# Optimization experiments

Measured on AMD Instinct MI355X. Metric: run time of the kernel, lower is better.

Reference implementation:

```python
import jax, jax.numpy as jnp
import numpy as np

N_VERTICES = 1_000_000
N_EDGES = 16_000_000


def setup_inputs() -> dict:
    key = jax.random.key(0)
    k1, k2, k3, k4 = jax.random.split(key, 4)
    # vertex_attr columns: [A_ii, b_i, x_i]; A_ii kept positive & away from 0
    A_ii = jax.random.uniform(k1, (N_VERTICES, 1), dtype=jnp.float32) + 0.5
    b_i = jax.random.normal(k2, (N_VERTICES, 1), dtype=jnp.float32)
    x_i = jax.random.normal(k3, (N_VERTICES, 1), dtype=jnp.float32)
    vertex_attr = jnp.concatenate([A_ii, b_i, x_i], axis=1)
    edgeij_pair = jax.random.randint(k4, (2, N_EDGES), 0, N_VERTICES, dtype=jnp.int64 if jax.config.read('jax_enable_x64') else jnp.int32)
    edge_attr = jax.random.normal(jax.random.fold_in(key, 5), (N_EDGES, 1), dtype=jnp.float32) * 0.05
    g = jnp.array([0.6667], dtype=jnp.float32)  # Jacobi damping weight w = g[0]
    batch = jnp.zeros((N_VERTICES,), dtype=edgeij_pair.dtype)  # single graph
    return {"vertex_attr": vertex_attr, "edgeij_pair": edgeij_pair,
            "edge_attr": edge_attr, "g": g, "batch": batch}


def reference(vertex_attr, edgeij_pair, edge_attr, g, batch):
    n = vertex_attr.shape[0]
    A_ii = vertex_attr[:, 0:1]  # [N,1]
    b_i = vertex_attr[:, 1:2]
    x_i = vertex_attr[:, 2:3]
    w = g[0]
    # edge-to-vertex scatter-sum aggregation: cbar_i = sum_{j in N(i)} c_ij
    dst = edgeij_pair[0]
    cbar_i = jax.ops.segment_sum(edge_attr[:, 0], dst, num_segments=n)[:, None]  # [N,1]
    # damped Jacobi update
    x_new = x_i + w * (b_i - cbar_i) / A_ii
    return jnp.concatenate([A_ii, b_i, x_new], axis=1)
```

## Files before the change

### kernel.cpp

```cpp
#include <hip/hip_runtime.h>

#define TPB    256
#define VSHIFT 12
#define VBUCK  (1 << VSHIFT)
#define NBMAX  256
#define EPT    16
#define ROUND  (TPB * EPT)
#define RPB    4
#define PBLK   (ROUND * RPB)
#define SPLITMAX 4
#define ATPB   1024
#define KDEP   8

#define FPSCALE20  1048576.0f
#define FPINV20    9.5367431640625e-7f

typedef unsigned uint32x4 __attribute__((ext_vector_type(4)));

__device__ __forceinline__ unsigned pack_edge(int d, float v) {
    int fix = __float2int_rn(v * FPSCALE20);
    return ((unsigned)(d & (VBUCK - 1)) << 20) | ((unsigned)fix & 0xFFFFFu);
}

__device__ __forceinline__ uint32x4 gload16_async(const void* p) {
    uint32x4 r;
    asm volatile("global_load_dwordx4 %0, %1, off"
                 : "=&v"(r) : "v"(p));
    return r;
}

__device__ __forceinline__ int block_excl_scan(int v, int t, int* wsum, int* total) {
    int s = v;
    #pragma unroll
    for (int d = 1; d < 64; d <<= 1) {
        int u = __shfl_up(s, d);
        if ((t & 63) >= d) s += u;
    }
    if ((t & 63) == 63) wsum[t >> 6] = s;
    __syncthreads();
    int add = 0;
    #pragma unroll
    for (int w = 0; w < TPB / 64; ++w)
        if (w < (t >> 6)) add += wsum[w];
    int tot = wsum[0] + wsum[1] + wsum[2] + wsum[3];
    __syncthreads();
    *total = tot;
    return s + add - v;
}

__global__ void hist_rounds_kernel(const int* __restrict__ dst, long long n_edge,
                                   int nblk, int* __restrict__ histp_t,
                                   int* __restrict__ histp_b) {
    __shared__ int h[NBMAX];
    const int t = threadIdx.x;
    const long long bbase = (long long)blockIdx.x * PBLK;
    int total = 0;
    for (int r = 0; r < RPB; ++r) {
        h[t] = 0;
        __syncthreads();
        const long long rbase = bbase + (long long)r * ROUND;
        #pragma unroll
        for (int j = 0; j < EPT / 4; ++j) {
            long long e = rbase + ((long long)j * TPB + t) * 4;
            if (e + 4 <= n_edge) {
                int4 d = *reinterpret_cast<const int4*>(dst + e);
                atomicAdd(&h[d.x >> VSHIFT], 1);
                atomicAdd(&h[d.y >> VSHIFT], 1);
                atomicAdd(&h[d.z >> VSHIFT], 1);
                atomicAdd(&h[d.w >> VSHIFT], 1);
            } else {
                for (int q = 0; q < 4; ++q) {
                    long long ee = e + q;
                    if (ee < n_edge) atomicAdd(&h[dst[ee] >> VSHIFT], 1);
                }
            }
        }
        __syncthreads();
        int hv = h[t];
        histp_t[((size_t)blockIdx.x * RPB + r) * NBMAX + t] = hv;
        total += hv;
    }
    histp_b[(size_t)t * nblk + blockIdx.x] = total;
}

__global__ void row_scan_kernel(int* __restrict__ histp, int nblk,
                                int* __restrict__ totals) {
    __shared__ int wsum[TPB / 64];
    const int t = threadIdx.x;
    int* row = histp + (size_t)blockIdx.x * nblk;
    int carry = 0;
    for (int base = 0; base < nblk; base += TPB) {
        int v = (base + t < nblk) ? row[base + t] : 0;
        int tot;
        int excl = block_excl_scan(v, t, wsum, &tot);
        if (base + t < nblk) row[base + t] = carry + excl;
        carry += tot;
        __syncthreads();
    }
    if (t == 0) totals[blockIdx.x] = carry;
}

__global__ void base_scan_kernel(const int* __restrict__ totals, int nb,
                                 int* __restrict__ base) {
    __shared__ int wsum[TPB / 64];
    const int t = threadIdx.x;
    int v = (t < nb) ? totals[t] : 0;
    int tot;
    int excl = block_excl_scan(v, t, wsum, &tot);
    base[t] = excl;
    if (t == TPB - 1) base[TPB] = excl + v;
}

__global__ __launch_bounds__(TPB, 7)
void partition_kernel(const int* __restrict__ dst,
                      const float* __restrict__ ea,
                      long long n_edge, int nblk,
                      const int* __restrict__ histp_t,
                      const int* __restrict__ histp_b,
                      const int* __restrict__ base,
                      unsigned* __restrict__ pairs) {
    __shared__ unsigned      stage[ROUND];
    __shared__ unsigned char stage_b[ROUND];
    __shared__ int pos[NBMAX];
    __shared__ int adj[NBMAX];
    __shared__ int wsum[TPB / 64];

    const int t = threadIdx.x;
    const long long bbase = (long long)blockIdx.x * PBLK;
    int my_gbase = base[t] + histp_b[(size_t)t * nblk + blockIdx.x];

    int hv[RPB];
    #pragma unroll
    for (int r = 0; r < RPB; ++r)
        hv[r] = histp_t[((size_t)blockIdx.x * RPB + r) * NBMAX + t];

    if (bbase + PBLK <= n_edge) {
        int4   dr[2][EPT / 4];
        float4 vr[2][EPT / 4];
        #pragma unroll
        for (int j = 0; j < EPT / 4; ++j) {
            long long e = bbase + ((long long)j * TPB + t) * 4;
            dr[0][j] = *reinterpret_cast<const int4*>(dst + e);
            vr[0][j] = *reinterpret_cast<const float4*>(ea + e);
        }
        #pragma unroll
        for (int r = 0; r < RPB; ++r) {
            const int cur = r & 1, nxt = cur ^ 1;
            if (r + 1 < RPB) {
                const long long pb = bbase + (long long)(r + 1) * ROUND;
                #pragma unroll
                for (int j = 0; j < EPT / 4; ++j) {
                    long long e = pb + ((long long)j * TPB + t) * 4;
                    dr[nxt][j] = *reinterpret_cast<const int4*>(dst + e);
                    vr[nxt][j] = *reinterpret_cast<const float4*>(ea + e);
                }
            }
            int rt;
            int excl = block_excl_scan(hv[r], t, wsum, &rt);
            pos[t] = excl;
            adj[t] = my_gbase - excl;
            __syncthreads();
            #pragma unroll
            for (int j = 0; j < EPT / 4; ++j) {
                int   dd[4] = {dr[cur][j].x, dr[cur][j].y, dr[cur][j].z, dr[cur][j].w};
                float vv[4] = {vr[cur][j].x, vr[cur][j].y, vr[cur][j].z, vr[cur][j].w};
                #pragma unroll
                for (int q = 0; q < 4; ++q) {
                    int b = dd[q] >> VSHIFT;
                    int slot = atomicAdd(&pos[b], 1);
                    stage[slot]   = pack_edge(dd[q], vv[q]);
                    stage_b[slot] = (unsigned char)b;
                }
            }
            __syncthreads();
            #pragma unroll
            for (int i0 = 0; i0 < ROUND; i0 += TPB) {
                int i = i0 + t;
                unsigned p = stage[i];
                int b = stage_b[i];
                pairs[(size_t)(adj[b] + i)] = p;
            }
            my_gbase += hv[r];
        }
    } else {
        const long long bend = n_edge;
        for (int r = 0; r < RPB; ++r) {
            const long long rbase = bbase + (long long)r * ROUND;
            if (rbase >= bend) break;

            int4   dreg[EPT / 4];
            float4 vreg[EPT / 4];
            int    nval[EPT / 4];
            #pragma unroll
            for (int j = 0; j < EPT / 4; ++j) {
                long long e = rbase + ((long long)j * TPB + t) * 4;
                if (e + 4 <= bend) {
                    dreg[j] = *reinterpret_cast<const int4*>(dst + e);
                    vreg[j] = *reinterpret_cast<const float4*>(ea + e);
                    nval[j] = 4;
                } else {
                    int dd[4] = {0, 0, 0, 0};
                    float vv[4] = {0.f, 0.f, 0.f, 0.f};
                    int nv = 0;
                    for (int q = 0; q < 4; ++q) {
                        long long ee = e + q;
                        if (ee < bend) { dd[q] = dst[ee]; vv[q] = ea[ee]; nv = q + 1; }
                    }
                    dreg[j] = make_int4(dd[0], dd[1], dd[2], dd[3]);
                    vreg[j] = make_float4(vv[0], vv[1], vv[2], vv[3]);
                    nval[j] = nv;
                }
            }

            int rt;
            int excl = block_excl_scan(hv[r], t, wsum, &rt);
            pos[t] = excl;
            adj[t] = my_gbase - excl;
            __syncthreads();

            #pragma unroll
            for (int j = 0; j < EPT / 4; ++j) {
                int   dd[4] = {dreg[j].x, dreg[j].y, dreg[j].z, dreg[j].w};
                float vv[4] = {vreg[j].x, vreg[j].y, vreg[j].z, vreg[j].w};
                #pragma unroll
                for (int q = 0; q < 4; ++q) {
                    if (q < nval[j]) {
                        int b = dd[q] >> VSHIFT;
                        int slot = atomicAdd(&pos[b], 1);
                        stage[slot]   = pack_edge(dd[q], vv[q]);
                        stage_b[slot] = (unsigned char)b;
                    }
                }
            }
            __syncthreads();

            for (int i = t; i < rt; i += TPB) {
                unsigned p = stage[i];
                int b = stage_b[i];
                pairs[(size_t)(adj[b] + i)] = p;
            }
            __syncthreads();
            my_gbase += hv[r];
        }
    }
}

__global__ __launch_bounds__(ATPB)
void accum_partial_kernel(const unsigned* pairs,
                          const int* __restrict__ base,
                          float* __restrict__ partials, int n_vert, int nb,
                          int split) {
    __shared__ __align__(16) int acc[VBUCK];
    const int b  = blockIdx.x % nb;
    const int sp = blockIdx.x / nb;
    const int t  = threadIdx.x;
    #pragma unroll
    for (int i = t; i < VBUCK; i += ATPB) acc[i] = 0;
    __syncthreads();

    const int s = base[b];
    const int e = base[b + 1];
    const long long len = e - s;
    const int i0 = s + (int)((len * sp) / split);
    const int i1 = s + (int)((len * (sp + 1)) / split);
    int a0 = (i0 + 3) & ~3;
    if (a0 > i1) a0 = i1;
    const int a1 = a0 + (((i1 - a0) >> 2) << 2);

    if (t == 0) {
        for (int i = i0; i < a0; ++i) {
            unsigned p = pairs[i];
            atomicAdd(&acc[(int)(p >> 20)], ((int)(p << 12)) >> 12);
        }
    }
    if (t == 1) {
        for (int i = a1; i < i1; ++i) {
            unsigned p = pairs[i];
            atomicAdd(&acc[(int)(p >> 20)], ((int)(p << 12)) >> 12);
        }
    }

    const int n4 = (a1 - a0) >> 2;
    if (n4 > 0) {
        const char* pv = reinterpret_cast<const char*>(pairs + a0);
        const int nm1 = n4 - 1;
        for (int bb = 0; bb < n4; bb += KDEP * ATPB) {
            uint32x4 q[KDEP];
            int idx[KDEP];
            #pragma unroll
            for (int k = 0; k < KDEP; ++k) {
                idx[k] = bb + t + k * ATPB;
                int ci = idx[k] < nm1 ? idx[k] : nm1;
                q[k] = gload16_async(pv + (size_t)ci * 16);
            }
            asm volatile("s_waitcnt vmcnt(0)" ::: "memory");
            __builtin_amdgcn_sched_barrier(0);
            #pragma unroll
            for (int k = 0; k < KDEP; ++k) {
                if (idx[k] < n4) {
                    #pragma unroll
                    for (int u = 0; u < 4; ++u) {
                        unsigned p = q[k][u];
                        atomicAdd(&acc[(int)(p >> 20)], ((int)(p << 12)) >> 12);
                    }
                }
            }
        }
    }
    __syncthreads();

    float* pp = partials + (size_t)sp * n_vert;
    const int vbase = b << VSHIFT;
    if (vbase + VBUCK <= n_vert) {
        int4 a = reinterpret_cast<const int4*>(acc)[t];
        float4 f;
        f.x = (float)a.x * FPINV20; f.y = (float)a.y * FPINV20;
        f.z = (float)a.z * FPINV20; f.w = (float)a.w * FPINV20;
        reinterpret_cast<float4*>(pp + vbase)[t] = f;
    } else {
        for (int v = t; vbase + v < n_vert; v += ATPB)
            pp[vbase + v] = (float)acc[v] * FPINV20;
    }
}

__global__ void final_update_kernel(const float* __restrict__ partials,
                                    const float* __restrict__ va,
                                    const float* __restrict__ g,
                                    float* __restrict__ out, int n_vert,
                                    int split) {
    const int gt = blockIdx.x * blockDim.x + threadIdx.x;
    const float w = g[0];
    const int v0 = gt * 4;
    if (v0 + 4 <= n_vert) {
        float4 c = reinterpret_cast<const float4*>(partials)[gt];
        for (int sp = 1; sp < split; ++sp) {
            float4 c2 = reinterpret_cast<const float4*>(
                            partials + (size_t)sp * n_vert)[gt];
            c.x += c2.x; c.y += c2.y; c.z += c2.z; c.w += c2.w;
        }
        float4 f0 = reinterpret_cast<const float4*>(va)[gt * 3 + 0];
        float4 f1 = reinterpret_cast<const float4*>(va)[gt * 3 + 1];
        float4 f2 = reinterpret_cast<const float4*>(va)[gt * 3 + 2];
        float4 o0, o1, o2;
        o0.x = f0.x; o0.y = f0.y; o0.z = f0.z + w * (f0.y - c.x) / f0.x;
        o0.w = f0.w; o1.x = f1.x; o1.y = f1.y + w * (f1.x - c.y) / f0.w;
        o1.z = f1.z; o1.w = f1.w; o2.x = f2.x + w * (f1.w - c.z) / f1.z;
        o2.y = f2.y; o2.z = f2.z; o2.w = f2.w + w * (f2.z - c.w) / f2.y;
        reinterpret_cast<float4*>(out)[gt * 3 + 0] = o0;
        reinterpret_cast<float4*>(out)[gt * 3 + 1] = o1;
        reinterpret_cast<float4*>(out)[gt * 3 + 2] = o2;
    } else {
        for (int i = v0; i < n_vert; ++i) {
            float c = 0.f;
            for (int sp = 0; sp < split; ++sp)
                c += partials[(size_t)sp * n_vert + i];
            float A = va[3 * i], bb = va[3 * i + 1], x = va[3 * i + 2];
            out[3 * i]     = A;
            out[3 * i + 1] = bb;
            out[3 * i + 2] = x + w * (bb - c) / A;
        }
    }
}

__global__ void accum_update_kernel(const unsigned* __restrict__ pairs,
                                    const int* __restrict__ base,
                                    const float* __restrict__ va,
                                    const float* __restrict__ g,
                                    float* __restrict__ out, int n_vert) {
    __shared__ __align__(16) int acc[VBUCK];
    const int b = blockIdx.x;
    const int T = blockDim.x;
    for (int t = threadIdx.x; t < VBUCK; t += T) acc[t] = 0;
    __syncthreads();
    const int s = base[b];
    const int e = base[b + 1];
    for (int i = s + threadIdx.x; i < e; i += T) {
        unsigned p = pairs[i];
        atomicAdd(&acc[(int)(p >> 20)], ((int)(p << 12)) >> 12);
    }
    __syncthreads();

    const float w = g[0];
    const int vbase = b << VSHIFT;
    const int t = threadIdx.x;
    const int v0 = vbase + t * 4;
    if (v0 + 4 <= n_vert) {
        const int gt = v0 >> 2;
        float4 f0 = reinterpret_cast<const float4*>(va)[gt * 3 + 0];
        float4 f1 = reinterpret_cast<const float4*>(va)[gt * 3 + 1];
        float4 f2 = reinterpret_cast<const float4*>(va)[gt * 3 + 2];
        int4   a  = reinterpret_cast<const int4*>(acc)[t];
        float4 c;
        c.x = (float)a.x * FPINV20; c.y = (float)a.y * FPINV20;
        c.z = (float)a.z * FPINV20; c.w = (float)a.w * FPINV20;
        float4 o0, o1, o2;
        o0.x = f0.x; o0.y = f0.y; o0.z = f0.z + w * (f0.y - c.x) / f0.x;
        o0.w = f0.w; o1.x = f1.x; o1.y = f1.y + w * (f1.x - c.y) / f0.w;
        o1.z = f1.z; o1.w = f1.w; o2.x = f2.x + w * (f1.w - c.z) / f1.z;
        o2.y = f2.y; o2.z = f2.z; o2.w = f2.w + w * (f2.z - c.w) / f2.y;
        reinterpret_cast<float4*>(out)[gt * 3 + 0] = o0;
        reinterpret_cast<float4*>(out)[gt * 3 + 1] = o1;
        reinterpret_cast<float4*>(out)[gt * 3 + 2] = o2;
    } else {
        for (int i = v0; i < n_vert && i < v0 + 4; ++i) {
            float A = va[3 * i], bb = va[3 * i + 1], x = va[3 * i + 2];
            out[3 * i]     = A;
            out[3 * i + 1] = bb;
            out[3 * i + 2] = x + w * (bb - (float)acc[i - vbase] * FPINV20) / A;
        }
    }
}

__global__ void scatter_add_dev_kernel(const int* __restrict__ dst,
                                       const float* __restrict__ ea,
                                       float* __restrict__ acc, int n_edges4) {
    int i = blockIdx.x * blockDim.x + threadIdx.x;
    const int stride = gridDim.x * blockDim.x;
    for (; i < n_edges4; i += stride) {
        int4   d = reinterpret_cast<const int4*>(dst)[i];
        float4 v = reinterpret_cast<const float4*>(ea)[i];
        atomicAdd(&acc[d.x], v.x);
        atomicAdd(&acc[d.y], v.y);
        atomicAdd(&acc[d.z], v.z);
        atomicAdd(&acc[d.w], v.w);
    }
}

__global__ void update_kernel(const float* __restrict__ va,
                              const float* __restrict__ cbar,
                              const float* __restrict__ g,
                              float* __restrict__ out, int n) {
    int i = blockIdx.x * blockDim.x + threadIdx.x;
    if (i >= n) return;
    float A = va[3 * i], b = va[3 * i + 1], x = va[3 * i + 2];
    out[3 * i]     = A;
    out[3 * i + 1] = b;
    out[3 * i + 2] = x + g[0] * (b - cbar[i]) / A;
}

extern "C" void kernel_launch(void* const* d_in, const int* in_sizes, int n_in,
                              void* d_out, int out_size, void* d_ws, size_t ws_size,
                              hipStream_t stream) {
    const float* vertex_attr = (const float*)d_in[0];
    const int*   edgeij      = (const int*)d_in[1];
    const float* edge_attr   = (const float*)d_in[2];
    const float* g           = (const float*)d_in[3];

    const int       n_vert = in_sizes[0] / 3;
    const long long n_edge = in_sizes[2];
    const int       nb     = (n_vert + VBUCK - 1) >> VSHIFT;
    const int       nblk   = (int)((n_edge + PBLK - 1) / PBLK);

    size_t histt_sz   = (size_t)nblk * RPB * NBMAX * sizeof(int);
    size_t histb_off  = (histt_sz + 255) & ~(size_t)255;
    size_t histb_sz   = (size_t)NBMAX * nblk * sizeof(int);
    size_t totals_off = (histb_off + histb_sz + 255) & ~(size_t)255;
    size_t base_off   = totals_off + NBMAX * sizeof(int);
    size_t pairs_off  = (base_off + (TPB + 1) * sizeof(int) + 255) & ~(size_t)255;
    size_t need1      = pairs_off + (size_t)n_edge * sizeof(unsigned);
    size_t part_off   = (need1 + 255) & ~(size_t)255;

    if (ws_size >= need1 && nb <= NBMAX) {
        int* histp_t = (int*)d_ws;
        int* histp_b = (int*)((char*)d_ws + histb_off);
        int* totals  = (int*)((char*)d_ws + totals_off);
        int* basep   = (int*)((char*)d_ws + base_off);
        unsigned* pairs = (unsigned*)((char*)d_ws + pairs_off);

        hist_rounds_kernel<<<nblk, TPB, 0, stream>>>(edgeij, n_edge, nblk,
                                                     histp_t, histp_b);
        row_scan_kernel<<<nb, TPB, 0, stream>>>(histp_b, nblk, totals);
        base_scan_kernel<<<1, TPB, 0, stream>>>(totals, nb, basep);
        partition_kernel<<<nblk, TPB, 0, stream>>>(edgeij, edge_attr, n_edge,
                                                   nblk, histp_t, histp_b,
                                                   basep, pairs);

        int split = 0;
        for (int sp = SPLITMAX; sp >= 2; sp >>= 1) {
            if (ws_size >= part_off + (size_t)sp * n_vert * sizeof(float)) {
                split = sp; break;
            }
        }
        if (split) {
            float* partials = (float*)((char*)d_ws + part_off);
            accum_partial_kernel<<<nb * split, ATPB, 0, stream>>>(
                pairs, basep, partials, n_vert, nb, split);
            const int uthreads = (n_vert + 3) / 4;
            final_update_kernel<<<(uthreads + TPB - 1) / TPB, TPB, 0, stream>>>(
                partials, vertex_attr, g, (float*)d_out, n_vert, split);
        } else {
            accum_update_kernel<<<nb, 1024, 0, stream>>>(pairs, basep, vertex_attr,
                                                         g, (float*)d_out, n_vert);
        }
    } else {
        float* cbar = (float*)d_ws;
        hipMemsetAsync(cbar, 0, (size_t)n_vert * sizeof(float), stream);
        scatter_add_dev_kernel<<<4096, TPB, 0, stream>>>(edgeij, edge_attr, cbar,
                                                         (int)(n_edge / 4));
        update_kernel<<<(n_vert + TPB - 1) / TPB, TPB, 0, stream>>>(
            vertex_attr, cbar, g, (float*)d_out, n_vert);
    }
}
```

Measured before the change: 127.0 us.

## Pad each bucket run in partitioned edge pairs to 8-element alignment

Each per-round, per-bucket segment of the partitioned pair array is rounded up to a multiple of 8 entries, and the gaps are filled with zero-valued dummy entries (packed 0 adds nothing to the accumulation). The aim is aligned 32-byte runs so that the scattered global writes and later reads of pairs are better coalesced or vector-aligned. In exchange the stage buffer grows (STG), occupancy hint drops from 7 to 5 blocks, the pairs array is larger, and the extra padding entries add memory traffic.

```diff
diff --git a/kernel.cpp b/kernel.cpp
--- a/kernel.cpp
+++ b/kernel.cpp
@@ -11,11 +11,17 @@
 #define SPLITMAX 4
 #define ATPB   1024
 #define KDEP   8
+#define PADE   8
+#define STG    5824
 
 #define FPSCALE20  1048576.0f
 #define FPINV20    9.5367431640625e-7f
 
 typedef unsigned uint32x4 __attribute__((ext_vector_type(4)));
+
+__device__ __host__ __forceinline__ int padup(int h) {
+    return h ? ((h + PADE - 1) & ~(PADE - 1)) : 0;
+}
 
 __device__ __forceinline__ unsigned pack_edge(int d, float v) {
     int fix = __float2int_rn(v * FPSCALE20);
@@ -78,7 +84,7 @@
         __syncthreads();
         int hv = h[t];
         histp_t[((size_t)blockIdx.x * RPB + r) * NBMAX + t] = hv;
-        total += hv;
+        total += padup(hv);
     }
     histp_b[(size_t)t * nblk + blockIdx.x] = total;
 }
@@ -111,7 +117,7 @@
     if (t == TPB - 1) base[TPB] = excl + v;
 }
 
-__global__ __launch_bounds__(TPB, 7)
+__global__ __launch_bounds__(TPB, 5)
 void partition_kernel(const int* __restrict__ dst,
                       const float* __restrict__ ea,
                       long long n_edge, int nblk,
@@ -119,8 +125,8 @@
                       const int* __restrict__ histp_b,
                       const int* __restrict__ base,
                       unsigned* __restrict__ pairs) {
-    __shared__ unsigned      stage[ROUND];
-    __shared__ unsigned char stage_b[ROUND];
+    __shared__ unsigned      stage[STG];
+    __shared__ unsigned char stage_b[STG];
     __shared__ int pos[NBMAX];
     __shared__ int adj[NBMAX];
     __shared__ int wsum[TPB / 64];
@@ -129,10 +135,12 @@
     const long long bbase = (long long)blockIdx.x * PBLK;
     int my_gbase = base[t] + histp_b[(size_t)t * nblk + blockIdx.x];
 
-    int hv[RPB];
+    int hv[RPB], phv[RPB];
     #pragma unroll
-    for (int r = 0; r < RPB; ++r)
-        hv[r] = histp_t[((size_t)blockIdx.x * RPB + r) * NBMAX + t];
+    for (int r = 0; r < RPB; ++r) {
+        hv[r]  = histp_t[((size_t)blockIdx.x * RPB + r) * NBMAX + t];
+        phv[r] = padup(hv[r]);
+    }
 
     if (bbase + PBLK <= n_edge) {
         int4   dr[2][EPT / 4];
@@ -156,7 +164,7 @@
                 }
             }
             int rt;
-            int excl = block_excl_scan(hv[r], t, wsum, &rt);
+            int excl = block_excl_scan(phv[r], t, wsum, &rt);
             pos[t] = excl;
             adj[t] = my_gbase - excl;
             __syncthreads();
@@ -172,15 +180,17 @@
                     stage_b[slot] = (unsigned char)b;
                 }
             }
+            for (int i = hv[r]; i < phv[r]; ++i) {
+                stage[excl + i]   = 0u;
+                stage_b[excl + i] = (unsigned char)t;
+            }
             __syncthreads();
-            #pragma unroll
-            for (int i0 = 0; i0 < ROUND; i0 += TPB) {
-                int i = i0 + t;
+            for (int i = t; i < rt; i += TPB) {
                 unsigned p = stage[i];
                 int b = stage_b[i];
                 pairs[(size_t)(adj[b] + i)] = p;
             }
-            my_gbase += hv[r];
+            my_gbase += phv[r];
         }
     } else {
         const long long bend = n_edge;
@@ -213,7 +223,7 @@
             }
 
             int rt;
-            int excl = block_excl_scan(hv[r], t, wsum, &rt);
+            int excl = block_excl_scan(phv[r], t, wsum, &rt);
             pos[t] = excl;
             adj[t] = my_gbase - excl;
             __syncthreads();
@@ -232,6 +242,10 @@
                     }
                 }
             }
+            for (int i = hv[r]; i < phv[r]; ++i) {
+                stage[excl + i]   = 0u;
+                stage_b[excl + i] = (unsigned char)t;
+            }
             __syncthreads();
 
             for (int i = t; i < rt; i += TPB) {
@@ -240,7 +254,7 @@
                 pairs[(size_t)(adj[b] + i)] = p;
             }
             __syncthreads();
-            my_gbase += hv[r];
+            my_gbase += phv[r];
         }
     }
 }
@@ -451,13 +465,15 @@
     const int       nb     = (n_vert + VBUCK - 1) >> VSHIFT;
     const int       nblk   = (int)((n_edge + PBLK - 1) / PBLK);
 
+    const long long pairs_cap = n_edge + (long long)nblk * RPB * NBMAX * (PADE - 1);
+
     size_t histt_sz   = (size_t)nblk * RPB * NBMAX * sizeof(int);
     size_t histb_off  = (histt_sz + 255) & ~(size_t)255;
     size_t histb_sz   = (size_t)NBMAX * nblk * sizeof(int);
     size_t totals_off = (histb_off + histb_sz + 255) & ~(size_t)255;
     size_t base_off   = totals_off + NBMAX * sizeof(int);
     size_t pairs_off  = (base_off + (TPB + 1) * sizeof(int) + 255) & ~(size_t)255;
-    size_t need1      = pairs_off + (size_t)n_edge * sizeof(unsigned);
+    size_t need1      = pairs_off + (size_t)pairs_cap * sizeof(unsigned);
     size_t part_off   = (need1 + 255) & ~(size_t)255;
 
     if (ws_size >= need1 && nb <= NBMAX) {
```

Measured after the change: 129.4 us. Within noise of the previous version (+2.0%).

## Widen vertex buckets to 16K and trade fixed-point bits for bucket index

Applied to the files above, without the earlier changes.

The vertex bucket grows from 4096 to 16384 vertices, so each packed edge word now holds a 14-bit local index and an 18-bit fixed-point value instead of 12 and 20. Fewer buckets mean fewer partition passes and blocks, and the split limit rises to 8 so each bucket can still be spread across enough blocks. The LDS accumulator grows to 64KB per block, which may reduce occupancy. The coarser 2^-18 quantization and smaller value range add precision risk on the edge values.

```diff
diff --git a/kernel.cpp b/kernel.cpp
--- a/kernel.cpp
+++ b/kernel.cpp
@@ -1,25 +1,25 @@
 #include <hip/hip_runtime.h>
 
 #define TPB    256
-#define VSHIFT 12
+#define VSHIFT 14
 #define VBUCK  (1 << VSHIFT)
 #define NBMAX  256
 #define EPT    16
 #define ROUND  (TPB * EPT)
 #define RPB    4
 #define PBLK   (ROUND * RPB)
-#define SPLITMAX 4
+#define SPLITMAX 8
 #define ATPB   1024
 #define KDEP   8
 
-#define FPSCALE20  1048576.0f
-#define FPINV20    9.5367431640625e-7f
+#define FPSCALE18  262144.0f
+#define FPINV18    3.814697265625e-6f
 
 typedef unsigned uint32x4 __attribute__((ext_vector_type(4)));
 
 __device__ __forceinline__ unsigned pack_edge(int d, float v) {
-    int fix = __float2int_rn(v * FPSCALE20);
-    return ((unsigned)(d & (VBUCK - 1)) << 20) | ((unsigned)fix & 0xFFFFFu);
+    int fix = __float2int_rn(v * FPSCALE18);
+    return ((unsigned)(d & (VBUCK - 1)) << 18) | ((unsigned)fix & 0x3FFFFu);
 }
 
 __device__ __forceinline__ uint32x4 gload16_async(const void* p) {
@@ -254,7 +254,6 @@
     const int b  = blockIdx.x % nb;
     const int sp = blockIdx.x / nb;
     const int t  = threadIdx.x;
-    #pragma unroll
     for (int i = t; i < VBUCK; i += ATPB) acc[i] = 0;
     __syncthreads();
 
@@ -270,13 +269,13 @@
     if (t == 0) {
         for (int i = i0; i < a0; ++i) {
             unsigned p = pairs[i];
-            atomicAdd(&acc[(int)(p >> 20)], ((int)(p << 12)) >> 12);
+            atomicAdd(&acc[(int)(p >> 18)], ((int)(p << 14)) >> 14);
         }
     }
     if (t == 1) {
         for (int i = a1; i < i1; ++i) {
             unsigned p = pairs[i];
-            atomicAdd(&acc[(int)(p >> 20)], ((int)(p << 12)) >> 12);
+            atomicAdd(&acc[(int)(p >> 18)], ((int)(p << 14)) >> 14);
         }
     }
 
@@ -301,7 +300,7 @@
                     #pragma unroll
                     for (int u = 0; u < 4; ++u) {
                         unsigned p = q[k][u];
-                        atomicAdd(&acc[(int)(p >> 20)], ((int)(p << 12)) >> 12);
+                        atomicAdd(&acc[(int)(p >> 18)], ((int)(p << 14)) >> 14);
                     }
                 }
             }
@@ -311,15 +310,18 @@
 
     float* pp = partials + (size_t)sp * n_vert;
     const int vbase = b << VSHIFT;
-    if (vbase + VBUCK <= n_vert) {
-        int4 a = reinterpret_cast<const int4*>(acc)[t];
-        float4 f;
-        f.x = (float)a.x * FPINV20; f.y = (float)a.y * FPINV20;
-        f.z = (float)a.z * FPINV20; f.w = (float)a.w * FPINV20;
-        reinterpret_cast<float4*>(pp + vbase)[t] = f;
-    } else {
-        for (int v = t; vbase + v < n_vert; v += ATPB)
-            pp[vbase + v] = (float)acc[v] * FPINV20;
+    for (int v4 = t * 4; v4 < VBUCK; v4 += ATPB * 4) {
+        int vi = vbase + v4;
+        if (vi + 4 <= n_vert) {
+            int4 a = *reinterpret_cast<const int4*>(&acc[v4]);
+            float4 f;
+            f.x = (float)a.x * FPINV18; f.y = (float)a.y * FPINV18;
+            f.z = (float)a.z * FPINV18; f.w = (float)a.w * FPINV18;
+            *reinterpret_cast<float4*>(pp + vi) = f;
+        } else {
+            for (int u = 0; u < 4; ++u)
+                if (vi + u < n_vert) pp[vi + u] = (float)acc[v4 + u] * FPINV18;
+        }
     }
 }
 
@@ -376,37 +378,42 @@
     const int e = base[b + 1];
     for (int i = s + threadIdx.x; i < e; i += T) {
         unsigned p = pairs[i];
-        atomicAdd(&acc[(int)(p >> 20)], ((int)(p << 12)) >> 12);
+        atomicAdd(&acc[(int)(p >> 18)], ((int)(p << 14)) >> 14);
     }
     __syncthreads();
 
     const float w = g[0];
     const int vbase = b << VSHIFT;
     const int t = threadIdx.x;
-    const int v0 = vbase + t * 4;
-    if (v0 + 4 <= n_vert) {
-        const int gt = v0 >> 2;
-        float4 f0 = reinterpret_cast<const float4*>(va)[gt * 3 + 0];
-        float4 f1 = reinterpret_cast<const float4*>(va)[gt * 3 + 1];
-        float4 f2 = reinterpret_cast<const float4*>(va)[gt * 3 + 2];
-        int4   a  = reinterpret_cast<const int4*>(acc)[t];
-        float4 c;
-        c.x = (float)a.x * FPINV20; c.y = (float)a.y * FPINV20;
-        c.z = (float)a.z * FPINV20; c.w = (float)a.w * FPINV20;
-        float4 o0, o1, o2;
-        o0.x = f0.x; o0.y = f0.y; o0.z = f0.z + w * (f0.y - c.x) / f0.x;
-        o0.w = f0.w; o1.x = f1.x; o1.y = f1.y + w * (f1.x - c.y) / f0.w;
-        o1.z = f1.z; o1.w = f1.w; o2.x = f2.x + w * (f1.w - c.z) / f1.z;
-        o2.y = f2.y; o2.z = f2.z; o2.w = f2.w + w * (f2.z - c.w) / f2.y;
-        reinterpret_cast<float4*>(out)[gt * 3 + 0] = o0;
-        reinterpret_cast<float4*>(out)[gt * 3 + 1] = o1;
-        reinterpret_cast<float4*>(out)[gt * 3 + 2] = o2;
-    } else {
-        for (int i = v0; i < n_vert && i < v0 + 4; ++i) {
-            float A = va[3 * i], bb = va[3 * i + 1], x = va[3 * i + 2];
-            out[3 * i]     = A;
-            out[3 * i + 1] = bb;
-            out[3 * i + 2] = x + w * (bb - (float)acc[i - vbase] * FPINV20) / A;
+    for (int v4 = t * 4; v4 < VBUCK; v4 += T * 4) {
+        int vi = vbase + v4;
+        if (vi + 4 <= n_vert) {
+            const int gt = vi >> 2;
+            float4 f0 = reinterpret_cast<const float4*>(va)[gt * 3 + 0];
+            float4 f1 = reinterpret_cast<const float4*>(va)[gt * 3 + 1];
+            float4 f2 = reinterpret_cast<const float4*>(va)[gt * 3 + 2];
+            int4   a  = *reinterpret_cast<const int4*>(&acc[v4]);
+            float4 c;
+            c.x = (float)a.x * FPINV18; c.y = (float)a.y * FPINV18;
+            c.z = (float)a.z * FPINV18; c.w = (float)a.w * FPINV18;
+            float4 o0, o1, o2;
+            o0.x = f0.x; o0.y = f0.y; o0.z = f0.z + w * (f0.y - c.x) / f0.x;
+            o0.w = f0.w; o1.x = f1.x; o1.y = f1.y + w * (f1.x - c.y) / f0.w;
+            o1.z = f1.z; o1.w = f1.w; o2.x = f2.x + w * (f1.w - c.z) / f1.z;
+            o2.y = f2.y; o2.z = f2.z; o2.w = f2.w + w * (f2.z - c.w) / f2.y;
+            reinterpret_cast<float4*>(out)[gt * 3 + 0] = o0;
+            reinterpret_cast<float4*>(out)[gt * 3 + 1] = o1;
+            reinterpret_cast<float4*>(out)[gt * 3 + 2] = o2;
+        } else {
+            for (int u = 0; u < 4; ++u) {
+                int i = vi + u;
+                if (i < n_vert) {
+                    float A = va[3 * i], bb = va[3 * i + 1], x = va[3 * i + 2];
+                    out[3 * i]     = A;
+                    out[3 * i + 1] = bb;
+                    out[3 * i + 2] = x + w * (bb - (float)acc[v4 + u] * FPINV18) / A;
+                }
+            }
         }
     }
 }
```

Result: faster. 113.7 us (-10.4%).
